# Kernel optimization log

Measured on AMD Instinct MI355X. Metric: run time of the kernel, lower is better.

Reference implementation:

```python
import jax, jax.numpy as jnp
import numpy as np

N_AGENTS = 8
S_DIM = 96
A_DIM = 32
ATT_DIM = 128   # attention_dim == hidden_dim of Attention
N_HEADS = 4
HEAD_DIM = ATT_DIM // N_HEADS
HIDDEN_1 = 128
SA_DIM = S_DIM + A_DIM  # 128, matches Attention in_dim
BATCH = 32768

leaky = lambda x: jax.nn.leaky_relu(x, negative_slope=0.01)


def setup_inputs() -> dict:
    key = jax.random.key(0)
    ks = jax.random.split(key, 18)
    sc = 0.05
    inp = {
        "s": jax.random.normal(ks[0], (BATCH, N_AGENTS * S_DIM), dtype=jnp.float32),
        "a": jax.random.uniform(ks[1], (BATCH, N_AGENTS * A_DIM), dtype=jnp.float32),
        # self agent (id=0) state encoder
        "W_enc_s": jax.random.normal(ks[2], (S_DIM, ATT_DIM), dtype=jnp.float32) * sc,
        "b_enc_s": jax.random.normal(ks[3], (ATT_DIM,), dtype=jnp.float32) * sc,
        # other agents' (1..7) distinct encoder_fc_sa weights, stacked
        "W_enc_sa": jax.random.normal(ks[4], (N_AGENTS - 1, SA_DIM, ATT_DIM), dtype=jnp.float32) * sc,
        "b_enc_sa": jax.random.normal(ks[5], (N_AGENTS - 1, ATT_DIM), dtype=jnp.float32) * sc,
        # attention block
        "Wq": jax.random.normal(ks[6], (ATT_DIM, ATT_DIM), dtype=jnp.float32) * sc,
        "Wk": jax.random.normal(ks[7], (ATT_DIM, ATT_DIM), dtype=jnp.float32) * sc,
        "Wv": jax.random.normal(ks[8], (ATT_DIM, ATT_DIM), dtype=jnp.float32) * sc,
        "bv": jax.random.normal(ks[9], (ATT_DIM,), dtype=jnp.float32) * sc,
        "Wo": jax.random.normal(ks[10], (ATT_DIM, ATT_DIM), dtype=jnp.float32) * sc,
        "bo": jax.random.normal(ks[11], (ATT_DIM,), dtype=jnp.float32) * sc,
        # head MLP
        "W_fc1": jax.random.normal(ks[12], (2 * ATT_DIM, HIDDEN_1), dtype=jnp.float32) * sc,
        "b_fc1": jax.random.normal(ks[13], (HIDDEN_1,), dtype=jnp.float32) * sc,
        "W_fc2": jax.random.normal(ks[14], (HIDDEN_1, A_DIM), dtype=jnp.float32) * sc,
        "b_fc2": jax.random.normal(ks[15], (A_DIM,), dtype=jnp.float32) * sc,
    }
    return inp


def reference(s, a, W_enc_s, b_enc_s, W_enc_sa, b_enc_sa,
              Wq, Wk, Wv, bv, Wo, bo, W_fc1, b_fc1, W_fc2, b_fc2):
    B = s.shape[0]
    n_other = N_AGENTS - 1

    # self agent (id=0) state encoding
    s_i_c = s[:, :S_DIM]                                   # [B, S]
    s_i = leaky(s_i_c @ W_enc_s + b_enc_s)                 # [B, D]

    # other agents' (state, action) slices -> per-agent linear + leakyrelu
    s_others = s[:, S_DIM:].reshape(B, n_other, S_DIM)     # [B, n, S]
    a_others = a[:, A_DIM:].reshape(B, n_other, A_DIM)     # [B, n, A]
    sa = jnp.concatenate([s_others, a_others], axis=-1)    # [B, n, S+A]
    e_k = leaky(jnp.einsum('bnf,nfd->bnd', sa, W_enc_sa) + b_enc_sa)  # [B, n, D]

    # multi-head attention: single query token (self), keys = other agents
    Q = (s_i @ Wq).reshape(B, N_HEADS, HEAD_DIM)                       # [B, H, d]
    K = jnp.einsum('bnd,de->bne', e_k, Wk).reshape(B, n_other, N_HEADS, HEAD_DIM)
    V = leaky(jnp.einsum('bnd,de->bne', e_k, Wv) + bv).reshape(B, n_other, N_HEADS, HEAD_DIM)
    scores = jnp.einsum('bhd,bnhd->bhn', Q, K) / np.sqrt(HEAD_DIM)     # [B, H, n]
    w = jax.nn.softmax(scores, axis=-1)
    attn = jnp.einsum('bhn,bnhd->bhd', w, V).reshape(B, ATT_DIM)       # [B, D]
    other_values = attn @ Wo + bo                                      # [B, D]

    # Q head
    X = jnp.concatenate([s_i, other_values], axis=1)       # [B, 2D]
    h = leaky(X @ W_fc1 + b_fc1)                           # [B, hidden_1]
    all_q = h @ W_fc2 + b_fc2                              # [B, A]

    int_acs = jnp.argmax(a[:, :A_DIM], axis=1, keepdims=True)   # [B, 1]
    q = jnp.take_along_axis(all_q, int_acs, axis=1)             # [B, 1]
    return (q, all_q)
```

## Files before the change

kernel.cpp:

```cpp
#include <hip/hip_runtime.h>
#include <math.h>


typedef __attribute__((ext_vector_type(8))) short bf16x8;
typedef __attribute__((ext_vector_type(4))) float f32x4;

#define PITCH 136
#define TRB 32

__device__ __forceinline__ float lrelu(float x){ return x > 0.f ? x : 0.01f * x; }

__device__ __forceinline__ unsigned short f2bf(float x){
    union { float f; unsigned u; } c; c.f = x;
    unsigned u = c.u; u += 0x7fffu + ((u >> 16) & 1u);
    return (unsigned short)(u >> 16);
}
__device__ __forceinline__ ushort4 pack4v(f32x4 v){
    ushort4 p; p.x = f2bf(v[0]); p.y = f2bf(v[1]); p.z = f2bf(v[2]); p.w = f2bf(v[3]);
    return p;
}
__device__ __forceinline__ f32x4 ldg_nt4(const float* p){
    return __builtin_nontemporal_load((const f32x4*)p);
}

__device__ __forceinline__ bf16x8 ldA(const unsigned short* __restrict__ WT, int Kc,
                                      int m0, int kc, int lane){
    return *(const bf16x8*)(WT + ((((size_t)(m0 >> 4)) * Kc + kc) << 9) + lane * 8);
}
__device__ __forceinline__ bf16x8 ldB(const unsigned short* L, int n0, int kc, int lane){
    return *(const bf16x8*)(L + (n0 + (lane & 15)) * PITCH + kc * 32 + (lane >> 4) * 8);
}

template<int NKC>
__device__ __forceinline__ void ldW(const unsigned short* __restrict__ WT, int Kc, int M0,
                                    int kc0, int lane, bf16x8 F[2][NKC]){
#pragma unroll
    for (int mt = 0; mt < 2; ++mt)
#pragma unroll
        for (int kc = 0; kc < NKC; ++kc)
            F[mt][kc] = ldA(WT, Kc, M0 + mt * 16, kc0 + kc, lane);
}

template<int NKC>
__device__ __forceinline__ void mmR(const bf16x8 F[2][NKC], const unsigned short* Ls,
                                    int lane, f32x4 acc[2][2]){
#pragma unroll
    for (int kc = 0; kc < NKC; ++kc) {
        bf16x8 b[2];
#pragma unroll
        for (int nt = 0; nt < 2; ++nt) b[nt] = ldB(Ls, nt * 16, kc, lane);
#pragma unroll
        for (int mt = 0; mt < 2; ++mt)
#pragma unroll
            for (int nt = 0; nt < 2; ++nt)
                acc[mt][nt] = __builtin_amdgcn_mfma_f32_16x16x32_bf16(F[mt][kc], b[nt], acc[mt][nt], 0, 0, 0);
    }
}

template<int NKC>
__device__ __forceinline__ void mmG(const unsigned short* __restrict__ WT, int Kc, int M0,
                                    int kc0, const unsigned short* Ls, int lane,
                                    f32x4 acc[2][2]){
    bf16x8 F[2][NKC];
    ldW<NKC>(WT, Kc, M0, kc0, lane, F);
    mmR<NKC>(F, Ls, lane, acc);
}

__device__ __forceinline__ void ld_sa_f(const float* __restrict__ s, const float* __restrict__ a,
                                        int row0, int n, int t, f32x4 sf[3], f32x4& af){
#pragma unroll
    for (int i = 0; i < 3; ++i) {
        int idx = t + 256 * i; int r = idx / 24, c4 = idx % 24;
        sf[i] = ldg_nt4(s + (size_t)(row0 + r) * 768 + 96 + 96 * n + c4 * 4);
    }
    af = ldg_nt4(a + (size_t)(row0 + (t >> 3)) * 256 + 32 + 32 * n + (t & 7) * 4);
}
__device__ __forceinline__ void st_sa(unsigned short* buf, int t,
                                      const f32x4 sf[3], const f32x4 af){
#pragma unroll
    for (int i = 0; i < 3; ++i) {
        int idx = t + 256 * i; int r = idx / 24, c4 = idx % 24;
        *(ushort4*)(buf + r * PITCH + c4 * 4) = pack4v(sf[i]);
    }
    *(ushort4*)(buf + (t >> 3) * PITCH + 96 + (t & 7) * 4) = pack4v(af);
}

__device__ __forceinline__ int froff(int q, int f, int Kc){
    return (((q >> 4) * Kc + (f >> 5)) << 9) + (((f >> 3) & 3) << 7) + ((q & 15) << 3) + (f & 7);
}

__global__ void wprep(const float* __restrict__ Ws, const float* __restrict__ Wsa,
                      const float* __restrict__ Wq_, const float* __restrict__ Wk_,
                      const float* __restrict__ Wv_, const float* __restrict__ Wo_,
                      const float* __restrict__ W1, const float* __restrict__ W2,
                      unsigned short* __restrict__ o)
{
    int id = blockIdx.x * 256 + threadIdx.x;
    if (id >= 229376) return;
    float v; int dst;
    if (id < 12288)        { int q = id / 96, f = id - q * 96;
                             v = Ws[f * 128 + q];              dst = froff(q, f, 3); }
    else if (id < 126976)  { int li = id - 12288; int n = li >> 14; int r = li & 16383;
                             int q = r >> 7, f = r & 127;
                             v = Wsa[n * 16384 + f * 128 + q]; dst = 12288 + n * 16384 + froff(q, f, 4); }
    else if (id < 143360)  { int li = id - 126976; int q = li >> 7, f = li & 127;
                             v = Wq_[f * 128 + q];             dst = 126976 + froff(q, f, 4); }
    else if (id < 159744)  { int li = id - 143360; int q = li >> 7, f = li & 127;
                             v = Wk_[f * 128 + q];             dst = 143360 + froff(q, f, 4); }
    else if (id < 176128)  { int li = id - 159744; int q = li >> 7, f = li & 127;
                             v = Wv_[f * 128 + q];             dst = 159744 + froff(q, f, 4); }
    else if (id < 192512)  { int li = id - 176128; int q = li >> 7, f = li & 127;
                             v = Wo_[f * 128 + q];             dst = 176128 + froff(q, f, 4); }
    else if (id < 225280)  { int li = id - 192512; int q = li >> 8, f = li & 255;
                             v = W1[f * 128 + q];              dst = 192512 + froff(q, f, 8); }
    else                   { int li = id - 225280; int q = li >> 7, f = li & 127;
                             v = W2[f * 32 + q];               dst = 225280 + froff(q, f, 4); }
    o[dst] = f2bf(v);
}

__global__ void __launch_bounds__(256, 2)
ac_mfma(const float* __restrict__ s, const float* __restrict__ a,
        const unsigned short* __restrict__ WS,
        const float* __restrict__ b_enc_s, const float* __restrict__ b_enc_sa,
        const float* __restrict__ bv, const float* __restrict__ bo,
        const float* __restrict__ b_fc1, const float* __restrict__ b_fc2,
        float* __restrict__ out_q, float* __restrict__ out_allq)
{
    __shared__ __align__(16) unsigned short SMEM[3 * TRB * PITCH];
    unsigned short* bufA = SMEM;
    unsigned short* sE   = SMEM + TRB * PITCH;
    unsigned short* sENC = SMEM + 2 * TRB * PITCH;

    const int t = threadIdx.x, lane = t & 63, wid = t >> 6;
    const int l15 = lane & 15, l4 = lane >> 4;
    const int M0 = 32 * wid;
    const int row0 = blockIdx.x * TRB;
    const float rsd = 0.17677669529663687f;

    const unsigned short* WencST = WS;
    const unsigned short* WsaT   = WS + 12288;
    const unsigned short* WqT    = WS + 126976;
    const unsigned short* WkT    = WS + 143360;
    const unsigned short* WvT    = WS + 159744;
    const unsigned short* WoT    = WS + 176128;
    const unsigned short* W1T    = WS + 192512;
    const unsigned short* W2T    = WS + 225280;

    f32x4 sf[3]; f32x4 af;

    ld_sa_f(s, a, row0, -1, t, sf, af);
    st_sa(bufA, t, sf, af);
    __syncthreads();

    f32x4 acc[2][2];
#pragma unroll
    for (int mt = 0; mt < 2; ++mt)
#pragma unroll
        for (int nt = 0; nt < 2; ++nt) acc[mt][nt] = (f32x4){0.f, 0.f, 0.f, 0.f};
    mmG<3>(WencST, 3, M0, 0, bufA, lane, acc);
    ld_sa_f(s, a, row0, 0, t, sf, af);
    __syncthreads();
#pragma unroll
    for (int mt = 0; mt < 2; ++mt) {
        float4 bb = *(const float4*)(b_enc_s + M0 + mt * 16 + l4 * 4);
#pragma unroll
        for (int nt = 0; nt < 2; ++nt) {
            f32x4 v;
            v[0] = lrelu(acc[mt][nt][0] + bb.x); v[1] = lrelu(acc[mt][nt][1] + bb.y);
            v[2] = lrelu(acc[mt][nt][2] + bb.z); v[3] = lrelu(acc[mt][nt][3] + bb.w);
            *(ushort4*)(sENC + (nt * 16 + l15) * PITCH + M0 + mt * 16 + l4 * 4) = pack4v(v);
        }
    }
    st_sa(bufA, t, sf, af);
    __syncthreads();

    f32x4 q[2][2];
#pragma unroll
    for (int mt = 0; mt < 2; ++mt)
#pragma unroll
        for (int nt = 0; nt < 2; ++nt) q[mt][nt] = (f32x4){0.f, 0.f, 0.f, 0.f};
    mmG<4>(WqT, 4, M0, 0, sENC, lane, q);

    float4 bvf[2];
#pragma unroll
    for (int mt = 0; mt < 2; ++mt) bvf[mt] = *(const float4*)(bv + M0 + mt * 16 + l4 * 4);

    f32x4 atn[2][2];
#pragma unroll
    for (int mt = 0; mt < 2; ++mt)
#pragma unroll
        for (int nt = 0; nt < 2; ++nt) atn[mt][nt] = (f32x4){0.f, 0.f, 0.f, 0.f};
    float m_[2] = {-INFINITY, -INFINITY}, l_[2] = {0.f, 0.f};

    for (int n = 0; n < 7; ++n) {
        f32x4 e[2][2];
#pragma unroll
        for (int mt = 0; mt < 2; ++mt)
#pragma unroll
            for (int nt = 0; nt < 2; ++nt) e[mt][nt] = (f32x4){0.f, 0.f, 0.f, 0.f};
        mmG<4>(WsaT + n * 16384, 4, M0, 0, bufA, lane, e);
        if (n < 6) ld_sa_f(s, a, row0, n + 1, t, sf, af);
        __syncthreads();

#pragma unroll
        for (int mt = 0; mt < 2; ++mt) {
            float4 bb = *(const float4*)(b_enc_sa + n * 128 + M0 + mt * 16 + l4 * 4);
#pragma unroll
            for (int nt = 0; nt < 2; ++nt) {
                f32x4 v;
                v[0] = lrelu(e[mt][nt][0] + bb.x); v[1] = lrelu(e[mt][nt][1] + bb.y);
                v[2] = lrelu(e[mt][nt][2] + bb.z); v[3] = lrelu(e[mt][nt][3] + bb.w);
                *(ushort4*)(sE + (nt * 16 + l15) * PITCH + M0 + mt * 16 + l4 * 4) = pack4v(v);
            }
        }
        if (n < 6) st_sa(bufA, t, sf, af);
        __syncthreads();

        f32x4 kv[2][2];
#pragma unroll
        for (int mt = 0; mt < 2; ++mt)
#pragma unroll
            for (int nt = 0; nt < 2; ++nt) kv[mt][nt] = (f32x4){0.f, 0.f, 0.f, 0.f};
        mmG<4>(WkT, 4, M0, 0, sE, lane, kv);

        float pr[2], corr[2];
#pragma unroll
        for (int nt = 0; nt < 2; ++nt) {
            float p = 0.f;
#pragma unroll
            for (int mt = 0; mt < 2; ++mt)
#pragma unroll
                for (int r = 0; r < 4; ++r) p = fmaf(q[mt][nt][r], kv[mt][nt][r], p);
            p += __shfl_xor(p, 16);
            p += __shfl_xor(p, 32);
            float sc = p * rsd;
            float mo = m_[nt], mn = fmaxf(mo, sc);
            pr[nt]   = __expf(sc - mn);
            corr[nt] = __expf(mo - mn);
            l_[nt] = l_[nt] * corr[nt] + pr[nt];
            m_[nt] = mn;
        }

#pragma unroll
        for (int mt = 0; mt < 2; ++mt)
#pragma unroll
            for (int nt = 0; nt < 2; ++nt) kv[mt][nt] = (f32x4){0.f, 0.f, 0.f, 0.f};
        mmG<4>(WvT, 4, M0, 0, sE, lane, kv);
#pragma unroll
        for (int mt = 0; mt < 2; ++mt)
#pragma unroll
            for (int nt = 0; nt < 2; ++nt)
#pragma unroll
                for (int r = 0; r < 4; ++r) {
                    float vv = lrelu(kv[mt][nt][r] + ((const float*)&bvf[mt])[r]);
                    atn[mt][nt][r] = fmaf(atn[mt][nt][r], corr[nt], pr[nt] * vv);
                }
    }

#pragma unroll
    for (int mt = 0; mt < 2; ++mt)
#pragma unroll
        for (int nt = 0; nt < 2; ++nt) {
            float inv = 1.f / l_[nt];
            f32x4 v;
            v[0] = atn[mt][nt][0] * inv; v[1] = atn[mt][nt][1] * inv;
            v[2] = atn[mt][nt][2] * inv; v[3] = atn[mt][nt][3] * inv;
            *(ushort4*)(bufA + (nt * 16 + l15) * PITCH + M0 + mt * 16 + l4 * 4) = pack4v(v);
        }
    __syncthreads();

#pragma unroll
    for (int mt = 0; mt < 2; ++mt)
#pragma unroll
        for (int nt = 0; nt < 2; ++nt) acc[mt][nt] = (f32x4){0.f, 0.f, 0.f, 0.f};
    mmG<4>(WoT, 4, M0, 0, bufA, lane, acc);
#pragma unroll
    for (int mt = 0; mt < 2; ++mt) {
        float4 bb = *(const float4*)(bo + M0 + mt * 16 + l4 * 4);
#pragma unroll
        for (int nt = 0; nt < 2; ++nt) {
            f32x4 v;
            v[0] = acc[mt][nt][0] + bb.x; v[1] = acc[mt][nt][1] + bb.y;
            v[2] = acc[mt][nt][2] + bb.z; v[3] = acc[mt][nt][3] + bb.w;
            *(ushort4*)(sE + (nt * 16 + l15) * PITCH + M0 + mt * 16 + l4 * 4) = pack4v(v);
        }
    }
    __syncthreads();

#pragma unroll
    for (int mt = 0; mt < 2; ++mt)
#pragma unroll
        for (int nt = 0; nt < 2; ++nt) acc[mt][nt] = (f32x4){0.f, 0.f, 0.f, 0.f};
    mmG<4>(W1T, 8, M0, 0, sENC, lane, acc);
    mmG<4>(W1T, 8, M0, 4, sE, lane, acc);
    __syncthreads();
#pragma unroll
    for (int mt = 0; mt < 2; ++mt) {
        float4 bb = *(const float4*)(b_fc1 + M0 + mt * 16 + l4 * 4);
#pragma unroll
        for (int nt = 0; nt < 2; ++nt) {
            f32x4 v;
            v[0] = lrelu(acc[mt][nt][0] + bb.x); v[1] = lrelu(acc[mt][nt][1] + bb.y);
            v[2] = lrelu(acc[mt][nt][2] + bb.z); v[3] = lrelu(acc[mt][nt][3] + bb.w);
            *(ushort4*)(bufA + (nt * 16 + l15) * PITCH + M0 + mt * 16 + l4 * 4) = pack4v(v);
        }
    }
    __syncthreads();

    float* P = (float*)(SMEM + TRB * PITCH);
    {
        bf16x8 a0 = ldA(W2T, 4, 0, wid, lane);
        bf16x8 a1 = ldA(W2T, 4, 16, wid, lane);
        bf16x8 b0 = ldB(bufA, 0, wid, lane);
        bf16x8 b1 = ldB(bufA, 16, wid, lane);
        f32x4 z = (f32x4){0.f, 0.f, 0.f, 0.f};
        f32x4 c00 = __builtin_amdgcn_mfma_f32_16x16x32_bf16(a0, b0, z, 0, 0, 0);
        f32x4 c01 = __builtin_amdgcn_mfma_f32_16x16x32_bf16(a0, b1, z, 0, 0, 0);
        f32x4 c10 = __builtin_amdgcn_mfma_f32_16x16x32_bf16(a1, b0, z, 0, 0, 0);
        f32x4 c11 = __builtin_amdgcn_mfma_f32_16x16x32_bf16(a1, b1, z, 0, 0, 0);
        *(f32x4*)(P + wid * 1024 + (l15     ) * 32 +      l4 * 4) = c00;
        *(f32x4*)(P + wid * 1024 + (16 + l15) * 32 +      l4 * 4) = c01;
        *(f32x4*)(P + wid * 1024 + (l15     ) * 32 + 16 + l4 * 4) = c10;
        *(f32x4*)(P + wid * 1024 + (16 + l15) * 32 + 16 + l4 * 4) = c11;
    }
    __syncthreads();

    float* S = (float*)SMEM;
#pragma unroll
    for (int j = 0; j < 4; ++j) {
        int o = t + 256 * j; int row = o >> 5, f = o & 31;
        float v = P[row * 32 + f] + P[1024 + row * 32 + f]
                + P[2048 + row * 32 + f] + P[3072 + row * 32 + f] + b_fc2[f];
        out_allq[(size_t)(row0 + row) * 32 + f] = v;
        S[row * 33 + f] = v;
    }
    __syncthreads();

    if (t < TRB) {
        int row = row0 + t;
        float best = -INFINITY; int bi = 0;
#pragma unroll
        for (int jj = 0; jj < 8; ++jj) {
            f32x4 v = ldg_nt4(a + (size_t)row * 256 + jj * 4);
#pragma unroll
            for (int e2 = 0; e2 < 4; ++e2)
                if (v[e2] > best) { best = v[e2]; bi = jj * 4 + e2; }
        }
        out_q[row] = S[t * 33 + bi];
    }
}

extern "C" void kernel_launch(void* const* d_in, const int* in_sizes, int n_in,
                              void* d_out, int out_size, void* d_ws, size_t ws_size,
                              hipStream_t stream)
{
    (void)n_in; (void)out_size; (void)ws_size;
    const float* s        = (const float*)d_in[0];
    const float* a        = (const float*)d_in[1];
    const float* W_enc_s  = (const float*)d_in[2];
    const float* b_enc_s  = (const float*)d_in[3];
    const float* W_enc_sa = (const float*)d_in[4];
    const float* b_enc_sa = (const float*)d_in[5];
    const float* Wq       = (const float*)d_in[6];
    const float* Wk       = (const float*)d_in[7];
    const float* Wv       = (const float*)d_in[8];
    const float* bv       = (const float*)d_in[9];
    const float* Wo       = (const float*)d_in[10];
    const float* bo       = (const float*)d_in[11];
    const float* W_fc1    = (const float*)d_in[12];
    const float* b_fc1    = (const float*)d_in[13];
    const float* W_fc2    = (const float*)d_in[14];
    const float* b_fc2    = (const float*)d_in[15];

    int B = in_sizes[0] / 768;
    float* out_q    = (float*)d_out;
    float* out_allq = out_q + B;
    unsigned short* WS = (unsigned short*)d_ws;

    wprep<<<dim3(896), dim3(256), 0, stream>>>(W_enc_s, W_enc_sa, Wq, Wk, Wv, Wo,
                                               W_fc1, W_fc2, WS);
    ac_mfma<<<dim3(B / TRB), dim3(256), 0, stream>>>(s, a, WS, b_enc_s, b_enc_sa,
                                                     bv, bo, b_fc1, b_fc2,
                                                     out_q, out_allq);
}
```

Before: 76.87 us.

## Double-buffer agent staging and overlap K/V phase with next encoder

Adds ping-pong shared buffers for the staged s/a inputs and for the encoded agent features. Each iteration now preloads encoder weights into registers and runs the K/V attention step for the previous agent before encoding the current one. This cuts the barriers per agent from two to one, and drops one barrier after the fc1 matmul. The cost is more shared memory per block (five tiles instead of three), which may press on occupancy, plus more live registers.

```diff
diff --git a/kernel.cpp b/kernel.cpp
--- a/kernel.cpp
+++ b/kernel.cpp
@@ -126,10 +126,12 @@
         const float* __restrict__ b_fc1, const float* __restrict__ b_fc2,
         float* __restrict__ out_q, float* __restrict__ out_allq)
 {
-    __shared__ __align__(16) unsigned short SMEM[3 * TRB * PITCH];
-    unsigned short* bufA = SMEM;
-    unsigned short* sE   = SMEM + TRB * PITCH;
-    unsigned short* sENC = SMEM + 2 * TRB * PITCH;
+    __shared__ __align__(16) unsigned short SMEM[5 * TRB * PITCH];
+    unsigned short* bufA0 = SMEM;
+    unsigned short* bufA1 = SMEM + TRB * PITCH;
+    unsigned short* sE0   = SMEM + 2 * TRB * PITCH;
+    unsigned short* sE1   = SMEM + 3 * TRB * PITCH;
+    unsigned short* sENC  = SMEM + 4 * TRB * PITCH;
 
     const int t = threadIdx.x, lane = t & 63, wid = t >> 6;
     const int l15 = lane & 15, l4 = lane >> 4;
@@ -149,7 +151,7 @@
     f32x4 sf[3]; f32x4 af;
 
     ld_sa_f(s, a, row0, -1, t, sf, af);
-    st_sa(bufA, t, sf, af);
+    st_sa(bufA0, t, sf, af);
     __syncthreads();
 
     f32x4 acc[2][2];
@@ -157,7 +159,7 @@
     for (int mt = 0; mt < 2; ++mt)
 #pragma unroll
         for (int nt = 0; nt < 2; ++nt) acc[mt][nt] = (f32x4){0.f, 0.f, 0.f, 0.f};
-    mmG<3>(WencST, 3, M0, 0, bufA, lane, acc);
+    mmG<3>(WencST, 3, M0, 0, bufA0, lane, acc);
     ld_sa_f(s, a, row0, 0, t, sf, af);
     __syncthreads();
 #pragma unroll
@@ -171,7 +173,7 @@
             *(ushort4*)(sENC + (nt * 16 + l15) * PITCH + M0 + mt * 16 + l4 * 4) = pack4v(v);
         }
     }
-    st_sa(bufA, t, sf, af);
+    st_sa(bufA1, t, sf, af);
     __syncthreads();
 
     f32x4 q[2][2];
@@ -192,37 +194,13 @@
         for (int nt = 0; nt < 2; ++nt) atn[mt][nt] = (f32x4){0.f, 0.f, 0.f, 0.f};
     float m_[2] = {-INFINITY, -INFINITY}, l_[2] = {0.f, 0.f};
 
-    for (int n = 0; n < 7; ++n) {
-        f32x4 e[2][2];
-#pragma unroll
-        for (int mt = 0; mt < 2; ++mt)
-#pragma unroll
-            for (int nt = 0; nt < 2; ++nt) e[mt][nt] = (f32x4){0.f, 0.f, 0.f, 0.f};
-        mmG<4>(WsaT + n * 16384, 4, M0, 0, bufA, lane, e);
-        if (n < 6) ld_sa_f(s, a, row0, n + 1, t, sf, af);
-        __syncthreads();
-
-#pragma unroll
-        for (int mt = 0; mt < 2; ++mt) {
-            float4 bb = *(const float4*)(b_enc_sa + n * 128 + M0 + mt * 16 + l4 * 4);
-#pragma unroll
-            for (int nt = 0; nt < 2; ++nt) {
-                f32x4 v;
-                v[0] = lrelu(e[mt][nt][0] + bb.x); v[1] = lrelu(e[mt][nt][1] + bb.y);
-                v[2] = lrelu(e[mt][nt][2] + bb.z); v[3] = lrelu(e[mt][nt][3] + bb.w);
-                *(ushort4*)(sE + (nt * 16 + l15) * PITCH + M0 + mt * 16 + l4 * 4) = pack4v(v);
-            }
-        }
-        if (n < 6) st_sa(bufA, t, sf, af);
-        __syncthreads();
-
-        f32x4 kv[2][2];
-#pragma unroll
-        for (int mt = 0; mt < 2; ++mt)
-#pragma unroll
-            for (int nt = 0; nt < 2; ++nt) kv[mt][nt] = (f32x4){0.f, 0.f, 0.f, 0.f};
-        mmG<4>(WkT, 4, M0, 0, sE, lane, kv);
-
+    auto kv_phase = [&](const unsigned short* EB){
+        f32x4 kk[2][2];
+#pragma unroll
+        for (int mt = 0; mt < 2; ++mt)
+#pragma unroll
+            for (int nt = 0; nt < 2; ++nt) kk[mt][nt] = (f32x4){0.f, 0.f, 0.f, 0.f};
+        mmG<4>(WkT, 4, M0, 0, EB, lane, kk);
         float pr[2], corr[2];
 #pragma unroll
         for (int nt = 0; nt < 2; ++nt) {
@@ -230,7 +208,7 @@
 #pragma unroll
             for (int mt = 0; mt < 2; ++mt)
 #pragma unroll
-                for (int r = 0; r < 4; ++r) p = fmaf(q[mt][nt][r], kv[mt][nt][r], p);
+                for (int r = 0; r < 4; ++r) p = fmaf(q[mt][nt][r], kk[mt][nt][r], p);
             p += __shfl_xor(p, 16);
             p += __shfl_xor(p, 32);
             float sc = p * rsd;
@@ -240,22 +218,56 @@
             l_[nt] = l_[nt] * corr[nt] + pr[nt];
             m_[nt] = mn;
         }
-
-#pragma unroll
-        for (int mt = 0; mt < 2; ++mt)
-#pragma unroll
-            for (int nt = 0; nt < 2; ++nt) kv[mt][nt] = (f32x4){0.f, 0.f, 0.f, 0.f};
-        mmG<4>(WvT, 4, M0, 0, sE, lane, kv);
+#pragma unroll
+        for (int mt = 0; mt < 2; ++mt)
+#pragma unroll
+            for (int nt = 0; nt < 2; ++nt) kk[mt][nt] = (f32x4){0.f, 0.f, 0.f, 0.f};
+        mmG<4>(WvT, 4, M0, 0, EB, lane, kk);
 #pragma unroll
         for (int mt = 0; mt < 2; ++mt)
 #pragma unroll
             for (int nt = 0; nt < 2; ++nt)
 #pragma unroll
                 for (int r = 0; r < 4; ++r) {
-                    float vv = lrelu(kv[mt][nt][r] + ((const float*)&bvf[mt])[r]);
+                    float vv = lrelu(kk[mt][nt][r] + ((const float*)&bvf[mt])[r]);
                     atn[mt][nt][r] = fmaf(atn[mt][nt][r], corr[nt], pr[nt] * vv);
                 }
-    }
+    };
+
+    for (int n = 0; n < 7; ++n) {
+        unsigned short* stageRd = (n & 1) ? bufA0 : bufA1;
+        unsigned short* stageWr = (n & 1) ? bufA1 : bufA0;
+        unsigned short* eWr     = (n & 1) ? sE1 : sE0;
+        unsigned short* eRd     = (n & 1) ? sE0 : sE1;
+
+        if (n < 6) ld_sa_f(s, a, row0, n + 1, t, sf, af);
+        bf16x8 F[2][4];
+        ldW<4>(WsaT + n * 16384, 4, M0, 0, lane, F);
+
+        if (n) kv_phase(eRd);
+
+        f32x4 e[2][2];
+#pragma unroll
+        for (int mt = 0; mt < 2; ++mt)
+#pragma unroll
+            for (int nt = 0; nt < 2; ++nt) e[mt][nt] = (f32x4){0.f, 0.f, 0.f, 0.f};
+        mmR<4>(F, stageRd, lane, e);
+
+#pragma unroll
+        for (int mt = 0; mt < 2; ++mt) {
+            float4 bb = *(const float4*)(b_enc_sa + n * 128 + M0 + mt * 16 + l4 * 4);
+#pragma unroll
+            for (int nt = 0; nt < 2; ++nt) {
+                f32x4 v;
+                v[0] = lrelu(e[mt][nt][0] + bb.x); v[1] = lrelu(e[mt][nt][1] + bb.y);
+                v[2] = lrelu(e[mt][nt][2] + bb.z); v[3] = lrelu(e[mt][nt][3] + bb.w);
+                *(ushort4*)(eWr + (nt * 16 + l15) * PITCH + M0 + mt * 16 + l4 * 4) = pack4v(v);
+            }
+        }
+        if (n < 6) st_sa(stageWr, t, sf, af);
+        __syncthreads();
+    }
+    kv_phase(sE0);
 
 #pragma unroll
     for (int mt = 0; mt < 2; ++mt)
@@ -265,7 +277,7 @@
             f32x4 v;
             v[0] = atn[mt][nt][0] * inv; v[1] = atn[mt][nt][1] * inv;
             v[2] = atn[mt][nt][2] * inv; v[3] = atn[mt][nt][3] * inv;
-            *(ushort4*)(bufA + (nt * 16 + l15) * PITCH + M0 + mt * 16 + l4 * 4) = pack4v(v);
+            *(ushort4*)(bufA0 + (nt * 16 + l15) * PITCH + M0 + mt * 16 + l4 * 4) = pack4v(v);
         }
     __syncthreads();
 
@@ -273,7 +285,7 @@
     for (int mt = 0; mt < 2; ++mt)
 #pragma unroll
         for (int nt = 0; nt < 2; ++nt) acc[mt][nt] = (f32x4){0.f, 0.f, 0.f, 0.f};
-    mmG<4>(WoT, 4, M0, 0, bufA, lane, acc);
+    mmG<4>(WoT, 4, M0, 0, bufA0, lane, acc);
 #pragma unroll
     for (int mt = 0; mt < 2; ++mt) {
         float4 bb = *(const float4*)(bo + M0 + mt * 16 + l4 * 4);
@@ -282,7 +294,7 @@
             f32x4 v;
             v[0] = acc[mt][nt][0] + bb.x; v[1] = acc[mt][nt][1] + bb.y;
             v[2] = acc[mt][nt][2] + bb.z; v[3] = acc[mt][nt][3] + bb.w;
-            *(ushort4*)(sE + (nt * 16 + l15) * PITCH + M0 + mt * 16 + l4 * 4) = pack4v(v);
+            *(ushort4*)(sE0 + (nt * 16 + l15) * PITCH + M0 + mt * 16 + l4 * 4) = pack4v(v);
         }
     }
     __syncthreads();
@@ -292,8 +304,7 @@
 #pragma unroll
         for (int nt = 0; nt < 2; ++nt) acc[mt][nt] = (f32x4){0.f, 0.f, 0.f, 0.f};
     mmG<4>(W1T, 8, M0, 0, sENC, lane, acc);
-    mmG<4>(W1T, 8, M0, 4, sE, lane, acc);
-    __syncthreads();
+    mmG<4>(W1T, 8, M0, 4, sE0, lane, acc);
 #pragma unroll
     for (int mt = 0; mt < 2; ++mt) {
         float4 bb = *(const float4*)(b_fc1 + M0 + mt * 16 + l4 * 4);
@@ -302,7 +313,7 @@
             f32x4 v;
             v[0] = lrelu(acc[mt][nt][0] + bb.x); v[1] = lrelu(acc[mt][nt][1] + bb.y);
             v[2] = lrelu(acc[mt][nt][2] + bb.z); v[3] = lrelu(acc[mt][nt][3] + bb.w);
-            *(ushort4*)(bufA + (nt * 16 + l15) * PITCH + M0 + mt * 16 + l4 * 4) = pack4v(v);
+            *(ushort4*)(bufA0 + (nt * 16 + l15) * PITCH + M0 + mt * 16 + l4 * 4) = pack4v(v);
         }
     }
     __syncthreads();
@@ -311,8 +322,8 @@
     {
         bf16x8 a0 = ldA(W2T, 4, 0, wid, lane);
         bf16x8 a1 = ldA(W2T, 4, 16, wid, lane);
-        bf16x8 b0 = ldB(bufA, 0, wid, lane);
-        bf16x8 b1 = ldB(bufA, 16, wid, lane);
+        bf16x8 b0 = ldB(bufA0, 0, wid, lane);
+        bf16x8 b1 = ldB(bufA0, 16, wid, lane);
         f32x4 z = (f32x4){0.f, 0.f, 0.f, 0.f};
         f32x4 c00 = __builtin_amdgcn_mfma_f32_16x16x32_bf16(a0, b0, z, 0, 0, 0);
         f32x4 c01 = __builtin_amdgcn_mfma_f32_16x16x32_bf16(a0, b1, z, 0, 0, 0);
@@ -325,7 +336,7 @@
     }
     __syncthreads();
 
-    float* S = (float*)SMEM;
+    float* S = (float*)sENC;
 #pragma unroll
     for (int j = 0; j < 4; ++j) {
         int o = t + 256 * j; int row = o >> 5, f = o & 31;
```

Measured after the change: 69.70 us. 1.1x faster.
